# Performance work log

Measured on AMD Instinct MI355X. Metric: run time of the kernel, lower is better.

The kernel has to match this reference:

```python
import jax, jax.numpy as jnp
import numpy as np

H, D, L = 4, 64, 7          # heads, hidden, seq_len (SEQ_LEN+2)
B = 32768                    # batch
VOCAB = 6
NOUT = 2 * 5 + 1             # 2*SEQ_LEN+1 = 11
EPS = 1e-5


def _ln(x, g, b):
    m = jnp.mean(x, axis=-1, keepdims=True)
    v = jnp.var(x, axis=-1, keepdims=True)
    return (x - m) / jnp.sqrt(v + EPS) * g + b


def _mha(q, k, v, wq, wk, wv, wo, bo):
    # wq/wk/wv: [H, D, D]; q: [B, Lq, D]; k,v: [B, Lk, D]
    qh = jnp.einsum('bqd,hde->hbqe', q, wq)
    kh = jnp.einsum('bkd,hde->hbke', k, wk)
    vh = jnp.einsum('bkd,hde->hbke', v, wv)
    s = jnp.einsum('hbqe,hbke->hbqk', qh, kh) / jnp.sqrt(jnp.asarray(D, q.dtype))
    # NOTE: original torch code softmaxes over dim=1 of [B,Lq,Lk] = the QUERY axis
    a = jax.nn.softmax(s, axis=2)
    o = jnp.einsum('hbqk,hbke->hbqe', a, vh)
    o = jnp.transpose(o, (1, 2, 0, 3)).reshape(q.shape[0], q.shape[1], H * D)
    return o @ wo + bo


def setup_inputs() -> dict:
    key = jax.random.key(0)
    ks = iter(jax.random.split(key, 32))
    n = lambda shape, s=0.02: jax.random.normal(next(ks), shape, dtype=jnp.float32) * s
    inp = {
        'tokens': jax.random.randint(next(ks), (B, L), 0, VOCAB, dtype=jnp.int32),
        'emb': n((VOCAB, D), 1.0),
        'pos': n((L, 1), 1.0),
        'qparam': n((1, D), 1.0),
        'in_w': n((D + 1, D)), 'in_b': n((D,)),
        # encoding layer (num_encoding_layers=1)
        'e_wq': n((H, D, D)), 'e_wk': n((H, D, D)), 'e_wv': n((H, D, D)),
        'e_wo': n((H * D, D)), 'e_bo': n((D,)),
        'e_g1': jnp.ones((D,), jnp.float32), 'e_b1': jnp.zeros((D,), jnp.float32),
        'e_c1w': n((D, 2 * D)), 'e_c1b': n((2 * D,)),
        'e_c2w': n((2 * D, D)), 'e_c2b': n((D,)),
        'e_g2': jnp.ones((D,), jnp.float32), 'e_b2': jnp.zeros((D,), jnp.float32),
        # decoder MHA
        'd_wq': n((H, D, D)), 'd_wk': n((H, D, D)), 'd_wv': n((H, D, D)),
        'd_wo': n((H * D, D)), 'd_bo': n((D,)),
        'fc_w': n((D, NOUT)), 'fc_b': n((NOUT,)),
    }
    return inp


def reference(tokens, emb, pos, qparam, in_w, in_b,
              e_wq, e_wk, e_wv, e_wo, e_bo, e_g1, e_b1,
              e_c1w, e_c1b, e_c2w, e_c2b, e_g2, e_b2,
              d_wq, d_wk, d_wv, d_wo, d_bo, fc_w, fc_b):
    x = emb[tokens]                                   # [B, L, D]
    p = jnp.broadcast_to(pos[None], (x.shape[0], L, 1))
    x = jnp.concatenate([x, p], axis=-1)              # [B, L, D+1]
    x = x @ in_w + in_b                               # Conv1d k=1 == linear
    # encoding layer
    x = _mha(x, x, x, e_wq, e_wk, e_wv, e_wo, e_bo)
    x = _ln(x, e_g1, e_b1)
    x1 = jax.nn.relu(x @ e_c1w + e_c1b)
    x1 = jax.nn.relu(x1 @ e_c2w + e_c2b)
    x = _ln(x + x1, e_g2, e_b2)
    # decoder: single learned query
    q = jnp.broadcast_to(qparam[None], (x.shape[0], 1, D))
    x = _mha(q, x, x, d_wq, d_wk, d_wv, d_wo, d_bo)   # [B, 1, D]
    x = x[:, 0, :]
    return x @ fc_w + fc_b                            # [B, 11]
```

## Files before the change

kernel.cpp:

```cpp
#include <hip/hip_runtime.h>
#include <hip/hip_bf16.h>

#define DEV __device__ __forceinline__

typedef __attribute__((ext_vector_type(8)))  short bf8v;
typedef __attribute__((ext_vector_type(16))) float f16v;
typedef __attribute__((ext_vector_type(4)))  float f4v;

static constexpr int NOUT = 11;

DEV unsigned short b16(float f){
  __hip_bfloat16 h = __float2bfloat16(f);
  unsigned short s; __builtin_memcpy(&s, &h, 2); return s;
}
DEV float bf2f(unsigned short s){
  __hip_bfloat16 h; __builtin_memcpy(&h, &s, 2); return __bfloat162float(h);
}
DEV unsigned pk2(float lo, float hi){
  return (unsigned)b16(lo) | ((unsigned)b16(hi) << 16);
}
template<bool BF16>
DEV float ldw(const void* p, int i){
  if constexpr (BF16) return bf2f(((const unsigned short*)p)[i]);
  else return ((const float*)p)[i];
}
DEV f16v MF(bf8v a, bf8v b, f16v c){
  return __builtin_amdgcn_mfma_f32_32x32x16_bf16(a, b, c, 0, 0, 0);
}
DEV f16v zf(){ f16v v;
  #pragma unroll
  for (int i=0;i<16;++i) v[i]=0.f;
  return v; }
DEV bf8v g16(const unsigned short* p){ return *(const bf8v*)p; }

struct PkTile { unsigned u[8]; };
DEV PkTile pack_tile(const f16v& a){
  PkTile t;
  #pragma unroll
  for (int j=0;j<8;++j) t.u[j] = pk2(a[2*j], a[2*j+1]);
  return t;
}
DEV bf8v as8(unsigned a, unsigned b, unsigned c, unsigned d){
  union { unsigned u[4]; bf8v v; } x;
  x.u[0]=a; x.u[1]=b; x.u[2]=c; x.u[3]=d; return x.v;
}
DEV void exch(const PkTile& t, int sub, bf8v& k0, bf8v& k1){
  unsigned sa = sub ? t.u[0] : t.u[2];
  unsigned sb = sub ? t.u[1] : t.u[3];
  unsigned sc = sub ? t.u[4] : t.u[6];
  unsigned sd = sub ? t.u[5] : t.u[7];
  unsigned ra = __shfl_xor(sa, 32);
  unsigned rb = __shfl_xor(sb, 32);
  unsigned rc = __shfl_xor(sc, 32);
  unsigned rd = __shfl_xor(sd, 32);
  if (sub == 0){
    k0 = as8(t.u[0], t.u[1], ra, rb);
    k1 = as8(t.u[4], t.u[5], rc, rd);
  } else {
    k0 = as8(ra, rb, t.u[2], t.u[3]);
    k1 = as8(rc, rd, t.u[6], t.u[7]);
  }
}


struct RawW {
  const void *in_w, *in_b, *pos;
  const void *e_wq, *e_wk, *e_wv, *e_wo, *e_bo;
  const void *g1, *b1, *c1w, *c1b, *c2w, *c2b, *g2, *b2;
  const void *d_wv, *d_wo, *d_bo, *fc_w, *fc_b;
};
struct PackP {
  unsigned short *Wt, *Mt, *Ut, *C1t, *C2t;
  float *BB, *WfT, *bfin;
};

template<bool BF16>
DEV void prep_impl(char* pbuf, int b, int t, const RawW r, PackP p){
  if (b < 8){
    const bool isM = (b < 4);
    const int h = isM ? b : b - 4;
    short* A_s = (short*)pbuf;
    short* B_s = A_s + 8448;
    const void* Araw = isM ? r.e_wq : r.e_wv;
    const void* Braw = isM ? r.e_wk : r.e_wo;
    for (int i = t; i < 4096; i += 512){
      A_s[(i>>6)*66 + (i&63)] = b16(ldw<BF16>(Araw, h*4096 + i));
      B_s[(i>>6)*66 + (i&63)] = b16(ldw<BF16>(Braw, h*4096 + i));
    }
    __syncthreads();
    unsigned short* dst = (isM ? p.Mt : p.Ut) + h*4096;
    const float scale = isM ? 0.125f : 1.0f;
    for (int idx = t; idx < 4096; idx += 512){
      int n = idx >> 6, k = idx & 63;
      float acc = 0.f;
      if (isM){
        #pragma unroll 8
        for (int e=0;e<64;++e)
          acc += bf2f(A_s[k*66+e]) * bf2f(B_s[n*66+e]);
      } else {
        #pragma unroll 8
        for (int e=0;e<64;++e)
          acc += bf2f(A_s[k*66+e]) * bf2f(B_s[e*66+n]);
      }
      dst[idx] = b16(acc * scale);
    }
  } else if (b == 8){
    short* c1s = (short*)pbuf;
    for (int i = t; i < 8192; i += 512)
      c1s[(i>>7)*130 + (i&127)] = b16(ldw<BF16>(r.c1w, i));
    __syncthreads();
    for (int idx = t; idx < 8192; idx += 512){
      int n = idx >> 6, k = idx & 63;
      p.C1t[idx] = c1s[k*130 + n];
    }
  } else if (b == 9){
    short* c2s = (short*)pbuf;
    for (int i = t; i < 8192; i += 512)
      c2s[(i>>6)*66 + (i&63)] = b16(ldw<BF16>(r.c2w, i));
    __syncthreads();
    for (int idx = t; idx < 8192; idx += 512){
      int n = idx >> 7, k = idx & 127;
      p.C2t[idx] = c2s[k*66 + n];
    }
  } else if (b == 10){
    short* ws = (short*)pbuf;
    for (int i = t; i < 4096; i += 512)
      ws[(i>>6)*66 + (i&63)] = b16(ldw<BF16>(r.in_w, i));
    __syncthreads();
    for (int idx = t; idx < 4096; idx += 512){
      int n = idx >> 6, k = idx & 63;
      p.Wt[idx] = ws[k*66 + n];
    }
  } else if (b == 11){
    for (int i = 0; i < 2; ++i){
      int idx = i*512 + t;
      float v;
      if (idx < 512){
        int l = idx >> 6, n = idx & 63;
        v = (l < 7) ? ldw<BF16>(r.in_b, n) + ldw<BF16>(r.pos, l) * ldw<BF16>(r.in_w, 64*64 + n)
                    : 0.f;
      } else {
        int q = idx - 512;
        if      (q < 64 ) v = ldw<BF16>(r.e_bo, q);
        else if (q < 192) v = ldw<BF16>(r.c1b, q-64);
        else if (q < 256) v = ldw<BF16>(r.c2b, q-192);
        else if (q < 320) v = ldw<BF16>(r.g1,  q-256);
        else if (q < 384) v = ldw<BF16>(r.b1,  q-320);
        else if (q < 448) v = ldw<BF16>(r.g2,  q-384);
        else              v = ldw<BF16>(r.b2,  q-448);
      }
      p.BB[idx] = v;
    }
  } else {
    short* Ws  = (short*)pbuf;
    float* G   = (float*)(pbuf + 33792);
    float* fcw = (float*)(pbuf + 45056);
    float* dbo = (float*)(pbuf + 47872);
    float* fcb = (float*)(pbuf + 48128);
    for (int i = t; i < 16384; i += 512) Ws[i] = b16(ldw<BF16>(r.d_wo, i));
    for (int i = t; i < 704;   i += 512) fcw[i] = ldw<BF16>(r.fc_w, i);
    if (t < 64) dbo[t] = ldw<BF16>(r.d_bo, t);
    if (t < 11) fcb[t] = ldw<BF16>(r.fc_b, t);
    __syncthreads();
    for (int g = t; g < 2816; g += 512){
      int he = g / 11, j = g - he*11;
      float acc = 0.f;
      #pragma unroll 8
      for (int ep=0; ep<64; ++ep)
        acc += bf2f(Ws[he*64+ep]) * fcw[ep*11+j];
      G[g] = acc;
    }
    __syncthreads();
    for (int i = t; i < 16384; i += 512)
      Ws[((i>>12)*64 + (i&63))*66 + ((i>>6)&63)] = b16(ldw<BF16>(r.d_wv, i));
    __syncthreads();
    for (int g = t; g < 715; g += 512){
      if (g < 704){
        int j = g >> 6, d = g & 63;
        float acc = 0.f;
        #pragma unroll 8
        for (int he=0; he<256; ++he)
          acc += bf2f(Ws[he*66 + d]) * G[he*11 + j];
        p.WfT[j*64 + d] = acc;
      } else {
        int j = g - 704;
        float acc = fcb[j];
        #pragma unroll 8
        for (int ep=0; ep<64; ++ep)
          acc += dbo[ep] * fcw[ep*11 + j];
        p.bfin[j] = acc;
      }
    }
  }
}
__global__ __launch_bounds__(512) void k_prep(RawW r, PackP p){
  __shared__ __align__(16) char pbuf[48192];
  bool bf = (*(const unsigned*)r.g1) != 0x3F800000u;
  if (bf) prep_impl<true >(pbuf, blockIdx.x, threadIdx.x, r, p);
  else    prep_impl<false>(pbuf, blockIdx.x, threadIdx.x, r, p);
}

struct KP {
  const int* tokens;
  const void* emb;
  const void* g1;
  const unsigned short *Wt, *Mt, *Ut, *C1t, *C2t;
  const float *BB, *WfT, *bfin;
  void* out;
};

__global__ __launch_bounds__(256, 4) void k_main(KP kp){
  __shared__ __align__(16) char smem[4*4096 + 4096 + 704];
  const int tid  = threadIdx.x;
  const int lane = tid & 63;
  const int wave = tid >> 6;
  const int l31  = lane & 31;
  const int sub  = lane >> 5;
  const int jm   = l31 >> 3;
  const bool isbf = (*(const unsigned*)kp.g1) != 0x3F800000u;

  float* Bpos  = (float*)(smem + 16384);
  float* biasf = Bpos + 512;
  char*  ostage = smem + 20480;
  #pragma unroll
  for (int i = tid; i < 1024; i += 256) Bpos[i] = kp.BB[i];

  short* Xw = (short*)(smem + wave*4096);
  const int item0 = (blockIdx.x*4 + wave)*4;

  {
    int c = lane & 7, pos = lane >> 3;
    #pragma unroll 1
    for (int it=0; it<4; ++it){
      int row = it*8 + pos;
      short* dst = Xw + row*64 + ((c ^ pos)*8);
      if (pos < 7){
        int tok = kp.tokens[(item0+it)*7 + pos];
        if (isbf){
          *(uint4*)dst = *(const uint4*)((const unsigned short*)kp.emb + tok*64 + c*8);
        } else {
          const float* e = (const float*)kp.emb + tok*64 + c*8;
          uint4 u;
          u.x = pk2(e[0], e[1]); u.y = pk2(e[2], e[3]);
          u.z = pk2(e[4], e[5]); u.w = pk2(e[6], e[7]);
          *(uint4*)dst = u;
        }
      } else {
        uint4 z; z.x=z.y=z.z=z.w=0u;
        *(uint4*)dst = z;
      }
    }
  }
  __syncthreads();

  bf8v xk[4];
  {
    f16v a0 = zf(), a1 = zf();
    #pragma unroll
    for (int s=0;s<4;++s){
      bf8v xb = *(const bf8v*)(Xw + l31*64 + (((2*s+sub) ^ (l31&7))*8));
      bf8v w0 = g16(kp.Wt + l31*64 + s*16 + sub*8);
      bf8v w1 = g16(kp.Wt + (32+l31)*64 + s*16 + sub*8);
      a0 = MF(w0, xb, a0);
      a1 = MF(w1, xb, a1);
    }
    const float* bp = Bpos + (l31 & 7)*64;
    #pragma unroll
    for (int run=0; run<4; ++run){
      f4v v0 = *(const f4v*)(bp + sub*4 + run*8);
      f4v v1 = *(const f4v*)(bp + 32 + sub*4 + run*8);
      #pragma unroll
      for (int q=0;q<4;++q){ a0[run*4+q] += v0[q]; a1[run*4+q] += v1[q]; }
    }
    PkTile px0 = pack_tile(a0), px1 = pack_tile(a1);
    exch(px0, sub, xk[0], xk[1]);
    exch(px1, sub, xk[2], xk[3]);
  }

  short* Pr = Xw;
  {
    uint4 z; z.x=z.y=z.z=z.w=0u;
    *(uint4*)(Pr + lane*16)     = z;
    *(uint4*)(Pr + lane*16 + 8) = z;
  }

  f16v o0, o1;
  {
    #pragma unroll
    for (int run=0; run<4; ++run){
      f4v v0 = *(const f4v*)(biasf + sub*4 + run*8);
      f4v v1 = *(const f4v*)(biasf + 32 + sub*4 + run*8);
      #pragma unroll
      for (int q=0;q<4;++q){ o0[run*4+q] = v0[q]; o1[run*4+q] = v1[q]; }
    }
  }
  #pragma unroll 1
  for (int h=0; h<4; ++h){
    const unsigned short* Mh = kp.Mt + h*4096;
    const unsigned short* Uh = kp.Ut + h*4096;
    f16v sc = zf();
    {
      f16v t0 = zf();
      #pragma unroll
      for (int s=0;s<4;++s){
        bf8v m0 = g16(Mh + l31*64 + s*16 + sub*8);
        t0 = MF(m0, xk[s], t0);
      }
      PkTile pt0 = pack_tile(t0);
      bf8v tA0, tA1;
      exch(pt0, sub, tA0, tA1);
      sc = MF(tA0, xk[0], sc);
      sc = MF(tA1, xk[1], sc);
    }
    {
      f16v t1 = zf();
      #pragma unroll
      for (int s=0;s<4;++s){
        bf8v m1 = g16(Mh + (32+l31)*64 + s*16 + sub*8);
        t1 = MF(m1, xk[s], t1);
      }
      PkTile pt1 = pack_tile(t1);
      bf8v tA2, tA3;
      exch(pt1, sub, tA2, tA3);
      sc = MF(tA2, xk[2], sc);
      sc = MF(tA3, xk[3], sc);
    }

    float s0=0.f, s1=0.f, s2=0.f, s3=0.f;
    #pragma unroll
    for (int r4=0;r4<4;++r4){
      if (r4 == jm){ s0=sc[r4*4+0]; s1=sc[r4*4+1]; s2=sc[r4*4+2]; s3=sc[r4*4+3]; }
    }
    float s3m = sub ? -3.0e38f : s3;
    float mx = fmaxf(fmaxf(s0,s1), fmaxf(s2,s3m));
    mx = fmaxf(mx, __shfl_xor(mx, 32));
    float e0=__expf(s0-mx), e1=__expf(s1-mx), e2=__expf(s2-mx);
    float e3 = sub ? 0.f : __expf(s3-mx);
    float sum = e0+e1+e2+e3;
    sum += __shfl_xor(sum, 32);
    float inv = 1.f/sum;
    float pv[4] = {e0*inv, e1*inv, e2*inv, e3*inv};
    #pragma unroll
    for (int i=0;i<4;++i){
      int q = jm*8 + 4*sub + i;
      Pr[q*32 + ((jm ^ i)*8) + (l31 & 7)] = (short)b16(pv[i]);
    }

    bf8v pb0 = *(const bf8v*)(Pr + l31*32 + (((sub  ) ^ (l31&3))*8));
    bf8v pb1 = *(const bf8v*)(Pr + l31*32 + (((2+sub) ^ (l31&3))*8));
    {
      f16v z0 = zf();
      #pragma unroll
      for (int s=0;s<4;++s){
        bf8v u0 = g16(Uh + l31*64 + s*16 + sub*8);
        z0 = MF(xk[s], u0, z0);
      }
      PkTile pz0 = pack_tile(z0);
      bf8v zA0, zA1;
      exch(pz0, sub, zA0, zA1);
      o0 = MF(zA0, pb0, o0);
      o0 = MF(zA1, pb1, o0);
    }
    {
      f16v z1 = zf();
      #pragma unroll
      for (int s=0;s<4;++s){
        bf8v u1 = g16(Uh + (32+l31)*64 + s*16 + sub*8);
        z1 = MF(xk[s], u1, z1);
      }
      PkTile pz1 = pack_tile(z1);
      bf8v zA2, zA3;
      exch(pz1, sub, zA2, zA3);
      o1 = MF(zA2, pb0, o1);
      o1 = MF(zA3, pb1, o1);
    }
  }

  f16v xl0, xl1;
  {
    float sm=0.f, sq=0.f;
    #pragma unroll
    for (int r=0;r<16;++r){ sm += o0[r]+o1[r]; sq += o0[r]*o0[r] + o1[r]*o1[r]; }
    sm += __shfl_xor(sm, 32);
    sq += __shfl_xor(sq, 32);
    float mean = sm * 0.015625f;
    float var  = sq * 0.015625f - mean*mean;
    float rs = rsqrtf(var + 1e-5f);
    const float* g1v = biasf + 256;
    const float* b1v = biasf + 320;
    #pragma unroll
    for (int run=0; run<4; ++run){
      f4v ga = *(const f4v*)(g1v + sub*4 + run*8);
      f4v ba = *(const f4v*)(b1v + sub*4 + run*8);
      f4v gb = *(const f4v*)(g1v + 32 + sub*4 + run*8);
      f4v bb = *(const f4v*)(b1v + 32 + sub*4 + run*8);
      #pragma unroll
      for (int q=0;q<4;++q){
        xl0[run*4+q] = (o0[run*4+q]-mean)*rs*ga[q] + ba[q];
        xl1[run*4+q] = (o1[run*4+q]-mean)*rs*gb[q] + bb[q];
      }
    }
  }
  PkTile pxl0 = pack_tile(xl0), pxl1 = pack_tile(xl1);
  bf8v hxk[4];
  exch(pxl0, sub, hxk[0], hxk[1]);
  exch(pxl1, sub, hxk[2], hxk[3]);

  f16v f2a = zf(), f2b = zf();
  #pragma unroll 1
  for (int hf=0; hf<2; ++hf){
    const float* c1b = biasf + 64 + hf*64;
    {
      f16v h0 = zf();
      #pragma unroll
      for (int s=0;s<4;++s){
        bf8v c0 = g16(kp.C1t + (hf*64 + l31)*64 + s*16 + sub*8);
        h0 = MF(c0, hxk[s], h0);
      }
      #pragma unroll
      for (int run=0; run<4; ++run){
        f4v v0 = *(const f4v*)(c1b + sub*4 + run*8);
        #pragma unroll
        for (int q=0;q<4;++q) h0[run*4+q] = fmaxf(h0[run*4+q]+v0[q], 0.f);
      }
      PkTile q0 = pack_tile(h0);
      bf8v hk0, hk1;
      exch(q0, sub, hk0, hk1);
      f2a = MF(g16(kp.C2t + l31*128       + hf*64 + 0*16 + sub*8), hk0, f2a);
      f2a = MF(g16(kp.C2t + l31*128       + hf*64 + 1*16 + sub*8), hk1, f2a);
      f2b = MF(g16(kp.C2t + (32+l31)*128  + hf*64 + 0*16 + sub*8), hk0, f2b);
      f2b = MF(g16(kp.C2t + (32+l31)*128  + hf*64 + 1*16 + sub*8), hk1, f2b);
    }
    {
      f16v h1 = zf();
      #pragma unroll
      for (int s=0;s<4;++s){
        bf8v c1 = g16(kp.C1t + (hf*64 + 32 + l31)*64 + s*16 + sub*8);
        h1 = MF(c1, hxk[s], h1);
      }
      #pragma unroll
      for (int run=0; run<4; ++run){
        f4v v1 = *(const f4v*)(c1b + 32 + sub*4 + run*8);
        #pragma unroll
        for (int q=0;q<4;++q) h1[run*4+q] = fmaxf(h1[run*4+q]+v1[q], 0.f);
      }
      PkTile q1 = pack_tile(h1);
      bf8v hk2, hk3;
      exch(q1, sub, hk2, hk3);
      f2a = MF(g16(kp.C2t + l31*128       + hf*64 + 2*16 + sub*8), hk2, f2a);
      f2a = MF(g16(kp.C2t + l31*128       + hf*64 + 3*16 + sub*8), hk3, f2a);
      f2b = MF(g16(kp.C2t + (32+l31)*128  + hf*64 + 2*16 + sub*8), hk2, f2b);
      f2b = MF(g16(kp.C2t + (32+l31)*128  + hf*64 + 3*16 + sub*8), hk3, f2b);
    }
  }

  float xf0[16], xf1[16];
  {
    const float* c2b = biasf + 192;
    #pragma unroll
    for (int run=0; run<4; ++run){
      f4v v0 = *(const f4v*)(c2b + sub*4 + run*8);
      f4v v1 = *(const f4v*)(c2b + 32 + sub*4 + run*8);
      #pragma unroll
      for (int q=0;q<4;++q){
        int r = run*4+q;
        float res0 = (r&1) ? bf2f((unsigned short)(pxl0.u[r>>1] >> 16))
                           : bf2f((unsigned short)(pxl0.u[r>>1] & 0xffffu));
        float res1 = (r&1) ? bf2f((unsigned short)(pxl1.u[r>>1] >> 16))
                           : bf2f((unsigned short)(pxl1.u[r>>1] & 0xffffu));
        xf0[r] = res0 + fmaxf(f2a[r] + v0[q], 0.f);
        xf1[r] = res1 + fmaxf(f2b[r] + v1[q], 0.f);
      }
    }
    float sm=0.f, sq=0.f;
    #pragma unroll
    for (int r=0;r<16;++r){ sm += xf0[r]+xf1[r]; sq += xf0[r]*xf0[r] + xf1[r]*xf1[r]; }
    sm += __shfl_xor(sm, 32);
    sq += __shfl_xor(sq, 32);
    float mean = sm * 0.015625f;
    float var  = sq * 0.015625f - mean*mean;
    float rs = rsqrtf(var + 1e-5f);
    const float* g2v = biasf + 384;
    const float* b2v = biasf + 448;
    #pragma unroll
    for (int run=0; run<4; ++run){
      f4v ga = *(const f4v*)(g2v + sub*4 + run*8);
      f4v ba = *(const f4v*)(b2v + sub*4 + run*8);
      f4v gb = *(const f4v*)(g2v + 32 + sub*4 + run*8);
      f4v bb = *(const f4v*)(b2v + 32 + sub*4 + run*8);
      #pragma unroll
      for (int q=0;q<4;++q){
        xf0[run*4+q] = (xf0[run*4+q]-mean)*rs*ga[q] + ba[q];
        xf1[run*4+q] = (xf1[run*4+q]-mean)*rs*gb[q] + bb[q];
      }
    }
  }

  if ((l31 & 7) == 7){
    #pragma unroll
    for (int r=0;r<16;++r){ xf0[r]=0.f; xf1[r]=0.f; }
  }
  #pragma unroll
  for (int r=0;r<16;++r){
    float v0 = xf0[r], v1 = xf1[r];
    v0 += __shfl_xor(v0,1); v0 += __shfl_xor(v0,2); v0 += __shfl_xor(v0,4);
    v1 += __shfl_xor(v1,1); v1 += __shfl_xor(v1,2); v1 += __shfl_xor(v1,4);
    xf0[r]=v0; xf1[r]=v1;
  }
  float* xsb = (float*)Pr;
  if ((l31 & 7) == 0){
    int it = l31 >> 3;
    #pragma unroll
    for (int run=0; run<4; ++run){
      f4v v0, v1;
      #pragma unroll
      for (int q=0;q<4;++q){ v0[q]=xf0[run*4+q]; v1[q]=xf1[run*4+q]; }
      *(f4v*)(xsb + it*64 + sub*4 + run*8) = v0;
      *(f4v*)(xsb + it*64 + 32 + sub*4 + run*8) = v1;
    }
  }
  if (lane < 44){
    int it = lane / 11, j = lane - it*11;
    float acc = kp.bfin[j];
    const float* xr = xsb + it*64;
    const float* wr = kp.WfT + j*64;
    #pragma unroll
    for (int k4=0;k4<64;k4+=4){
      f4v xv = *(const f4v*)(xr + k4);
      f4v wv = *(const f4v*)(wr + k4);
      acc += xv[0]*wv[0]+xv[1]*wv[1]+xv[2]*wv[2]+xv[3]*wv[3];
    }
    int slot = (wave*4 + it)*NOUT + j;
    if (isbf) ((unsigned short*)ostage)[slot] = b16(acc);
    else      ((float*)ostage)[slot] = acc;
  }
  __syncthreads();
  if (isbf){
    if (tid < 88)
      ((unsigned*)kp.out)[blockIdx.x*88 + tid] = ((const unsigned*)ostage)[tid];
  } else {
    if (tid < 176)
      ((unsigned*)kp.out)[blockIdx.x*176 + tid] = ((const unsigned*)ostage)[tid];
  }
}

extern "C" void kernel_launch(void* const* d_in, const int* in_sizes, int n_in,
                              void* d_out, int out_size, void* d_ws, size_t ws_size,
                              hipStream_t stream){
  const int* tokens = (const int*)d_in[0];
  const void* emb = d_in[1];
  const void* g1  = d_in[11];
  RawW r { d_in[4], d_in[5], d_in[2],
           d_in[6], d_in[7], d_in[8], d_in[9], d_in[10],
           d_in[11], d_in[12], d_in[13], d_in[14], d_in[15], d_in[16], d_in[17], d_in[18],
           d_in[21], d_in[22], d_in[23], d_in[24], d_in[25] };

  char* ws = (char*)d_ws;
  float* BB   = (float*)(ws + 0);
  float* WfT  = (float*)(ws + 4096);
  float* bfin = (float*)(ws + 6912);
  unsigned short* Wt  = (unsigned short*)(ws + 8192);
  unsigned short* Mt  = (unsigned short*)(ws + 16384);
  unsigned short* Ut  = (unsigned short*)(ws + 49152);
  unsigned short* C1t = (unsigned short*)(ws + 81920);
  unsigned short* C2t = (unsigned short*)(ws + 98304);

  PackP p { Wt, Mt, Ut, C1t, C2t, BB, WfT, bfin };
  k_prep<<<13, 512, 0, stream>>>(r, p);

  KP kp { tokens, emb, g1, Wt, Mt, Ut, C1t, C2t, BB, WfT, bfin, d_out };
  k_main<<<2048, 256, 0, stream>>>(kp);
}
```

Measured before the change: 235.5 us.

## Keep activations in per-wave LDS instead of registers and drop block syncs

Activation fragments (xk, hxk) no longer sit in registers; they are stored to a swizzled per-wave LDS buffer and re-read as MFMA operands, which should cut VGPR pressure and allow launch bounds of 6 waves per SIMD. Bias/pos tables are read straight from global memory rather than staged in LDS, and both __syncthreads are removed because each wave works only on its own LDS region. The output staging buffer goes away in favour of direct scattered global stores. The cost is extra LDS traffic on every MFMA and less coalesced output writes.

```diff
diff --git a/kernel.cpp b/kernel.cpp
--- a/kernel.cpp
+++ b/kernel.cpp
@@ -60,6 +60,19 @@
     k0 = as8(ra, rb, t.u[2], t.u[3]);
     k1 = as8(rc, rd, t.u[6], t.u[7]);
   }
+}
+
+DEV void store_swz(short* Xs, int l31, int sub, const PkTile& t, int ft){
+  #pragma unroll
+  for (int run=0; run<4; ++run){
+    int phys = (ft*4 + run) ^ (l31 & 7);
+    uint2 v; v.x = t.u[run*2]; v.y = t.u[run*2+1];
+    *(uint2*)(Xs + l31*64 + phys*8 + sub*4) = v;
+  }
+}
+DEV bf8v read_frag(const short* Xs, int l31, int sub, int s){
+  int phys = (2*s + sub) ^ (l31 & 7);
+  return *(const bf8v*)(Xs + l31*64 + phys*8);
 }
 
 
@@ -209,8 +222,8 @@
   void* out;
 };
 
-__global__ __launch_bounds__(256, 4) void k_main(KP kp){
-  __shared__ __align__(16) char smem[4*4096 + 4096 + 704];
+__global__ __launch_bounds__(256, 6) void k_main(KP kp){
+  __shared__ __align__(16) char smem[4*6144];
   const int tid  = threadIdx.x;
   const int lane = tid & 63;
   const int wave = tid >> 6;
@@ -219,13 +232,11 @@
   const int jm   = l31 >> 3;
   const bool isbf = (*(const unsigned*)kp.g1) != 0x3F800000u;
 
-  float* Bpos  = (float*)(smem + 16384);
-  float* biasf = Bpos + 512;
-  char*  ostage = smem + 20480;
-  #pragma unroll
-  for (int i = tid; i < 1024; i += 256) Bpos[i] = kp.BB[i];
-
-  short* Xw = (short*)(smem + wave*4096);
+  const float* BB    = kp.BB;
+  const float* biasf = BB + 512;
+
+  short* Xs = (short*)(smem + wave*6144);
+  short* Pr = Xs + 2048;
   const int item0 = (blockIdx.x*4 + wave)*4;
 
   {
@@ -233,7 +244,7 @@
     #pragma unroll 1
     for (int it=0; it<4; ++it){
       int row = it*8 + pos;
-      short* dst = Xw + row*64 + ((c ^ pos)*8);
+      short* dst = Xs + row*64 + ((c ^ pos)*8);
       if (pos < 7){
         int tok = kp.tokens[(item0+it)*7 + pos];
         if (isbf){
@@ -251,20 +262,16 @@
       }
     }
   }
-  __syncthreads();
-
-  bf8v xk[4];
+
   {
     f16v a0 = zf(), a1 = zf();
     #pragma unroll
     for (int s=0;s<4;++s){
-      bf8v xb = *(const bf8v*)(Xw + l31*64 + (((2*s+sub) ^ (l31&7))*8));
-      bf8v w0 = g16(kp.Wt + l31*64 + s*16 + sub*8);
-      bf8v w1 = g16(kp.Wt + (32+l31)*64 + s*16 + sub*8);
-      a0 = MF(w0, xb, a0);
-      a1 = MF(w1, xb, a1);
-    }
-    const float* bp = Bpos + (l31 & 7)*64;
+      bf8v xb = read_frag(Xs, l31, sub, s);
+      a0 = MF(g16(kp.Wt + l31*64      + s*16 + sub*8), xb, a0);
+      a1 = MF(g16(kp.Wt + (32+l31)*64 + s*16 + sub*8), xb, a1);
+    }
+    const float* bp = BB + (l31 & 7)*64;
     #pragma unroll
     for (int run=0; run<4; ++run){
       f4v v0 = *(const f4v*)(bp + sub*4 + run*8);
@@ -273,11 +280,10 @@
       for (int q=0;q<4;++q){ a0[run*4+q] += v0[q]; a1[run*4+q] += v1[q]; }
     }
     PkTile px0 = pack_tile(a0), px1 = pack_tile(a1);
-    exch(px0, sub, xk[0], xk[1]);
-    exch(px1, sub, xk[2], xk[3]);
-  }
-
-  short* Pr = Xw;
+    store_swz(Xs, l31, sub, px0, 0);
+    store_swz(Xs, l31, sub, px1, 1);
+  }
+
   {
     uint4 z; z.x=z.y=z.z=z.w=0u;
     *(uint4*)(Pr + lane*16)     = z;
@@ -302,28 +308,24 @@
     {
       f16v t0 = zf();
       #pragma unroll
-      for (int s=0;s<4;++s){
-        bf8v m0 = g16(Mh + l31*64 + s*16 + sub*8);
-        t0 = MF(m0, xk[s], t0);
-      }
+      for (int s=0;s<4;++s)
+        t0 = MF(g16(Mh + l31*64 + s*16 + sub*8), read_frag(Xs, l31, sub, s), t0);
       PkTile pt0 = pack_tile(t0);
       bf8v tA0, tA1;
       exch(pt0, sub, tA0, tA1);
-      sc = MF(tA0, xk[0], sc);
-      sc = MF(tA1, xk[1], sc);
+      sc = MF(tA0, read_frag(Xs, l31, sub, 0), sc);
+      sc = MF(tA1, read_frag(Xs, l31, sub, 1), sc);
     }
     {
       f16v t1 = zf();
       #pragma unroll
-      for (int s=0;s<4;++s){
-        bf8v m1 = g16(Mh + (32+l31)*64 + s*16 + sub*8);
-        t1 = MF(m1, xk[s], t1);
-      }
+      for (int s=0;s<4;++s)
+        t1 = MF(g16(Mh + (32+l31)*64 + s*16 + sub*8), read_frag(Xs, l31, sub, s), t1);
       PkTile pt1 = pack_tile(t1);
       bf8v tA2, tA3;
       exch(pt1, sub, tA2, tA3);
-      sc = MF(tA2, xk[2], sc);
-      sc = MF(tA3, xk[3], sc);
+      sc = MF(tA2, read_frag(Xs, l31, sub, 2), sc);
+      sc = MF(tA3, read_frag(Xs, l31, sub, 3), sc);
     }
 
     float s0=0.f, s1=0.f, s2=0.f, s3=0.f;
@@ -351,10 +353,8 @@
     {
       f16v z0 = zf();
       #pragma unroll
-      for (int s=0;s<4;++s){
-        bf8v u0 = g16(Uh + l31*64 + s*16 + sub*8);
-        z0 = MF(xk[s], u0, z0);
-      }
+      for (int s=0;s<4;++s)
+        z0 = MF(read_frag(Xs, l31, sub, s), g16(Uh + l31*64 + s*16 + sub*8), z0);
       PkTile pz0 = pack_tile(z0);
       bf8v zA0, zA1;
       exch(pz0, sub, zA0, zA1);
@@ -364,10 +364,8 @@
     {
       f16v z1 = zf();
       #pragma unroll
-      for (int s=0;s<4;++s){
-        bf8v u1 = g16(Uh + (32+l31)*64 + s*16 + sub*8);
-        z1 = MF(xk[s], u1, z1);
-      }
+      for (int s=0;s<4;++s)
+        z1 = MF(read_frag(Xs, l31, sub, s), g16(Uh + (32+l31)*64 + s*16 + sub*8), z1);
       PkTile pz1 = pack_tile(z1);
       bf8v zA2, zA3;
       exch(pz1, sub, zA2, zA3);
@@ -376,7 +374,6 @@
     }
   }
 
-  f16v xl0, xl1;
   {
     float sm=0.f, sq=0.f;
     #pragma unroll
@@ -388,6 +385,7 @@
     float rs = rsqrtf(var + 1e-5f);
     const float* g1v = biasf + 256;
     const float* b1v = biasf + 320;
+    f16v xl0, xl1;
     #pragma unroll
     for (int run=0; run<4; ++run){
       f4v ga = *(const f4v*)(g1v + sub*4 + run*8);
@@ -400,11 +398,10 @@
         xl1[run*4+q] = (o1[run*4+q]-mean)*rs*gb[q] + bb[q];
       }
     }
-  }
-  PkTile pxl0 = pack_tile(xl0), pxl1 = pack_tile(xl1);
-  bf8v hxk[4];
-  exch(pxl0, sub, hxk[0], hxk[1]);
-  exch(pxl1, sub, hxk[2], hxk[3]);
+    PkTile pxl0 = pack_tile(xl0), pxl1 = pack_tile(xl1);
+    store_swz(Xs, l31, sub, pxl0, 0);
+    store_swz(Xs, l31, sub, pxl1, 1);
+  }
 
   f16v f2a = zf(), f2b = zf();
   #pragma unroll 1
@@ -413,10 +410,9 @@
     {
       f16v h0 = zf();
       #pragma unroll
-      for (int s=0;s<4;++s){
-        bf8v c0 = g16(kp.C1t + (hf*64 + l31)*64 + s*16 + sub*8);
-        h0 = MF(c0, hxk[s], h0);
-      }
+      for (int s=0;s<4;++s)
+        h0 = MF(g16(kp.C1t + (hf*64 + l31)*64 + s*16 + sub*8),
+                read_frag(Xs, l31, sub, s), h0);
       #pragma unroll
       for (int run=0; run<4; ++run){
         f4v v0 = *(const f4v*)(c1b + sub*4 + run*8);
@@ -434,10 +430,9 @@
     {
       f16v h1 = zf();
       #pragma unroll
-      for (int s=0;s<4;++s){
-        bf8v c1 = g16(kp.C1t + (hf*64 + 32 + l31)*64 + s*16 + sub*8);
-        h1 = MF(c1, hxk[s], h1);
-      }
+      for (int s=0;s<4;++s)
+        h1 = MF(g16(kp.C1t + (hf*64 + 32 + l31)*64 + s*16 + sub*8),
+                read_frag(Xs, l31, sub, s), h1);
       #pragma unroll
       for (int run=0; run<4; ++run){
         f4v v1 = *(const f4v*)(c1b + 32 + sub*4 + run*8);
@@ -461,16 +456,16 @@
     for (int run=0; run<4; ++run){
       f4v v0 = *(const f4v*)(c2b + sub*4 + run*8);
       f4v v1 = *(const f4v*)(c2b + 32 + sub*4 + run*8);
-      #pragma unroll
-      for (int q=0;q<4;++q){
-        int r = run*4+q;
-        float res0 = (r&1) ? bf2f((unsigned short)(pxl0.u[r>>1] >> 16))
-                           : bf2f((unsigned short)(pxl0.u[r>>1] & 0xffffu));
-        float res1 = (r&1) ? bf2f((unsigned short)(pxl1.u[r>>1] >> 16))
-                           : bf2f((unsigned short)(pxl1.u[r>>1] & 0xffffu));
-        xf0[r] = res0 + fmaxf(f2a[r] + v0[q], 0.f);
-        xf1[r] = res1 + fmaxf(f2b[r] + v1[q], 0.f);
-      }
+      uint2 r0 = *(const uint2*)(Xs + l31*64 + ((0*4+run) ^ (l31&7))*8 + sub*4);
+      uint2 r1 = *(const uint2*)(Xs + l31*64 + ((1*4+run) ^ (l31&7))*8 + sub*4);
+      xf0[run*4+0] = bf2f((unsigned short)(r0.x & 0xffffu)) + fmaxf(f2a[run*4+0] + v0[0], 0.f);
+      xf0[run*4+1] = bf2f((unsigned short)(r0.x >> 16))     + fmaxf(f2a[run*4+1] + v0[1], 0.f);
+      xf0[run*4+2] = bf2f((unsigned short)(r0.y & 0xffffu)) + fmaxf(f2a[run*4+2] + v0[2], 0.f);
+      xf0[run*4+3] = bf2f((unsigned short)(r0.y >> 16))     + fmaxf(f2a[run*4+3] + v0[3], 0.f);
+      xf1[run*4+0] = bf2f((unsigned short)(r1.x & 0xffffu)) + fmaxf(f2b[run*4+0] + v1[0], 0.f);
+      xf1[run*4+1] = bf2f((unsigned short)(r1.x >> 16))     + fmaxf(f2b[run*4+1] + v1[1], 0.f);
+      xf1[run*4+2] = bf2f((unsigned short)(r1.y & 0xffffu)) + fmaxf(f2b[run*4+2] + v1[2], 0.f);
+      xf1[run*4+3] = bf2f((unsigned short)(r1.y >> 16))     + fmaxf(f2b[run*4+3] + v1[3], 0.f);
     }
     float sm=0.f, sq=0.f;
     #pragma unroll
@@ -530,17 +525,9 @@
       f4v wv = *(const f4v*)(wr + k4);
       acc += xv[0]*wv[0]+xv[1]*wv[1]+xv[2]*wv[2]+xv[3]*wv[3];
     }
-    int slot = (wave*4 + it)*NOUT + j;
-    if (isbf) ((unsigned short*)ostage)[slot] = b16(acc);
-    else      ((float*)ostage)[slot] = acc;
-  }
-  __syncthreads();
-  if (isbf){
-    if (tid < 88)
-      ((unsigned*)kp.out)[blockIdx.x*88 + tid] = ((const unsigned*)ostage)[tid];
-  } else {
-    if (tid < 176)
-      ((unsigned*)kp.out)[blockIdx.x*176 + tid] = ((const unsigned*)ostage)[tid];
+    int gi = item0 + it;
+    if (isbf) ((__hip_bfloat16*)kp.out)[gi*NOUT+j] = __float2bfloat16(acc);
+    else      ((float*)kp.out)[gi*NOUT+j] = acc;
   }
 }
 
```

Measured after the change: 370.7 us. 57.4% more time.
